# Kernel optimization log

Hardware: AMD Instinct MI355X
Metric: run time of the kernel (lower is better)

## Reference

```python
import jax, jax.numpy as jnp
import numpy as np

B, H, S, D, KG = 1, 8, 1024, 64, 10

def setup_inputs() -> dict:
    key = jax.random.key(0)
    ks = jax.random.split(key, 16)
    n = jax.random.normal
    u = jax.random.uniform
    return {
        'Q': n(ks[0], (B, H, S, D), dtype=jnp.float32),
        'K': n(ks[1], (B, H, S, D), dtype=jnp.float32),
        'V': n(ks[2], (B, H, S, D), dtype=jnp.float32),
        'distance_matrix': u(ks[3], (B, H, S, S), dtype=jnp.float32) * 10.0,
        'energy_matrix': u(ks[4], (B, H, S, S), dtype=jnp.float32) * 5.0,
        'mask': jnp.ones((B, H, S, S), dtype=jnp.int32),
        'mu_D': n(ks[5], (KG,), dtype=jnp.float32),
        'sigma_D': u(ks[6], (KG,), dtype=jnp.float32) + 0.5,  # keep sigma positive
        'b_D': n(ks[7], (KG,), dtype=jnp.float32) * 0.1,
        'mu_E': n(ks[8], (KG,), dtype=jnp.float32),
        'sigma_E': u(ks[9], (KG,), dtype=jnp.float32) + 0.5,
        'b_E': n(ks[10], (KG,), dtype=jnp.float32) * 0.1,
        'W1': n(ks[11], (KG, KG), dtype=jnp.float32) / np.sqrt(KG),
        'b1': jnp.zeros((KG,), dtype=jnp.float32),
        'W2': n(ks[12], (1, KG), dtype=jnp.float32) / np.sqrt(KG),
        'b2': jnp.zeros((1,), dtype=jnp.float32),
    }


def _rbf_mlp_bias(x, b, mu, sigma, W1, b1, W2, b2):
    # x: [B,H,S,S] -> Gaussian RBF features over K kernels, then small MLP -> [B,H,S,S]
    z = (x[..., None] + b - mu) / sigma                      # [B,H,S,S,K]
    inv_norm = 1.0 / (jnp.sqrt(2.0 * jnp.pi) * sigma)
    psi = jnp.exp(-0.5 * z * z) * inv_norm                   # [B,H,S,S,K]
    h = jax.nn.gelu(jnp.einsum('bhijk,lk->bhijl', psi, W1) + b1, approximate=False)
    return (jnp.einsum('bhijk,lk->bhijl', h, W2) + b2)[..., 0]


def reference(Q, K, V, distance_matrix, energy_matrix, mask,
              mu_D, sigma_D, b_D, mu_E, sigma_E, b_E, W1, b1, W2, b2):
    d_model = Q.shape[-1]
    scores = jnp.einsum('bhid,bhjd->bhij', Q, K) / np.sqrt(d_model * 2)
    scores = scores + _rbf_mlp_bias(distance_matrix, b_D, mu_D, sigma_D, W1, b1, W2, b2)
    scores = scores + _rbf_mlp_bias(energy_matrix, b_E, mu_E, sigma_E, W1, b1, W2, b2)
    scores = jnp.where(mask == 0, jnp.float32(-1e9), scores)
    attn = jax.nn.softmax(scores, axis=-1)
    return jnp.einsum('bhij,bhjd->bhid', attn, V)
```

## Files before the change

### kernel.cpp

```cpp
#include <hip/hip_runtime.h>
#include <math.h>

#define Hn 8
#define Sn 1024
#define Dn 64
#define KG 10

#define TN 2048
#define RD 10.25f
#define RE 5.125f

typedef __attribute__((ext_vector_type(8))) short bf16x8;
typedef __attribute__((ext_vector_type(4))) float f32x4;
typedef unsigned short u16;
typedef unsigned int u32;

__device__ inline float bf2f(u16 u) {
    union { u32 i; float f; } v;
    v.i = ((u32)u) << 16;
    return v.f;
}

__device__ inline u16 f2bf(float f) {
    union { float f; u32 i; } v;
    v.f = f;
    u32 i = v.i;
    return (u16)((i + 0x7FFFu + ((i >> 16) & 1u)) >> 16);
}

__device__ float bias_eval(float x,
                           const float* __restrict__ mu, const float* __restrict__ sg,
                           const float* __restrict__ bb,
                           const float* __restrict__ W1, const float* __restrict__ b1,
                           const float* __restrict__ W2, const float* __restrict__ b2) {
    const float inv_s2pi = 0.39894228040143267794f;
    float psi[KG];
#pragma unroll
    for (int k = 0; k < KG; k++) {
        float s = sg[k];
        float z = (x + bb[k] - mu[k]) / s;
        psi[k] = __expf(-0.5f * z * z) * (inv_s2pi / s);
    }
    float out = b2[0];
#pragma unroll
    for (int l = 0; l < KG; l++) {
        float a = b1[l];
#pragma unroll
        for (int k = 0; k < KG; k++) a += psi[k] * W1[l * KG + k];
        float g = 0.5f * a * (1.0f + erff(a * 0.70710678118654752440f));
        out += g * W2[l];
    }
    return out;
}

#define QK4 262144
#define VTN 524288

__global__ __launch_bounds__(256) void prep_kernel(
    const float* __restrict__ Q, const float* __restrict__ K, const float* __restrict__ V,
    const float* __restrict__ muD, const float* __restrict__ sgD, const float* __restrict__ bD,
    const float* __restrict__ muE, const float* __restrict__ sgE, const float* __restrict__ bE,
    const float* __restrict__ W1, const float* __restrict__ b1,
    const float* __restrict__ W2, const float* __restrict__ b2,
    u32* __restrict__ tab, u16* __restrict__ Qb, u16* __restrict__ Kb, u16* __restrict__ VTi)
{
    int id = blockIdx.x * 256 + threadIdx.x;
    if (id < 2 * TN) {
        int which = (id >= TN);
        int idx = id & (TN - 1);
        float h = (which ? RE : RD) / (float)TN;
        float x0 = idx * h;
        float v0, v1;
        if (which) {
            v0 = bias_eval(x0,     muE, sgE, bE, W1, b1, W2, b2);
            v1 = bias_eval(x0 + h, muE, sgE, bE, W1, b1, W2, b2);
        } else {
            v0 = bias_eval(x0,     muD, sgD, bD, W1, b1, W2, b2);
            v1 = bias_eval(x0 + h, muD, sgD, bD, W1, b1, W2, b2);
        }
        tab[id] = (u32)f2bf(v0) | ((u32)f2bf(v1 - v0) << 16);
    } else if (id < 2 * TN + QK4) {
        int i = id - 2 * TN;
        int arr = i >> 17;
        i &= (1 << 17) - 1;
        float4 v = ((const float4*)(arr ? K : Q))[i];
        ushort4 o;
        o.x = f2bf(v.x); o.y = f2bf(v.y); o.z = f2bf(v.z); o.w = f2bf(v.w);
        ((ushort4*)(arr ? Kb : Qb))[i] = o;
    } else if (id < 2 * TN + QK4 + VTN) {
        int g = id - (2 * TN + QK4);
        int h = g >> 16;
        int d = (g >> 10) & 63;
        int s = g & 1023;
        int t = s >> 5, q = (s >> 3) & 3, j = s & 7;
        int src_s = (t << 5) + (q << 2) + (j & 3) + ((j >> 2) << 4);
        VTi[g] = f2bf(V[(((size_t)h << 10) + src_s) * Dn + d]);
    }
}

__device__ inline float lerp_tab(const u32* __restrict__ st, float x, float invh) {
    float tf = x * invh;
    int i = (int)tf;
    i = max(0, min(i, TN - 1));
    float fr = tf - (float)i;
    u32 p = st[i];
    return fmaf(bf2f((u16)(p >> 16)), fr, bf2f((u16)p));
}

__global__ __launch_bounds__(256) void attn_kernel(
    const u16* __restrict__ Qb, const u16* __restrict__ Kb, const u16* __restrict__ VTi,
    const float* __restrict__ Dm, const float* __restrict__ Em, const int* __restrict__ Mk,
    const u32* __restrict__ gtab, float* __restrict__ out)
{
    __shared__ __align__(16) u32 sTab[2 * TN];
    __shared__ float sO[4][16][68];
    __shared__ float sM[4][16], sL[4][16];

    const int tid = threadIdx.x;
    {
        const uint4* g4 = (const uint4*)gtab;
        uint4* s4 = (uint4*)sTab;
#pragma unroll
        for (int i = 0; i < 4; i++) s4[tid + 256 * i] = g4[tid + 256 * i];
    }
    __syncthreads();

    const int h    = blockIdx.y;
    const int q0   = blockIdx.x * 16;
    const int wave = tid >> 6;
    const int lane = tid & 63;
    const int quad = lane >> 4;
    const int l16  = lane & 15;

    const u16* Qh = Qb  + (size_t)h * Sn * Dn;
    const u16* Kh = Kb  + (size_t)h * Sn * Dn;
    const u16* Vh = VTi + (size_t)h * Dn * Sn;
    const float* Dh = Dm + (size_t)h * Sn * Sn + (size_t)(q0 + l16) * Sn;
    const float* Eh = Em + (size_t)h * Sn * Sn + (size_t)(q0 + l16) * Sn;
    const int*   Mh = Mk + (size_t)h * Sn * Sn + (size_t)(q0 + l16) * Sn;
    const float invhD = (float)TN / RD;
    const float invhE = (float)TN / RE;
    const float scale = 0.08838834764831845f;

    const bf16x8 bQ0 = *(const bf16x8*)(Qh + (q0 + l16) * Dn + quad * 8);
    const bf16x8 bQ1 = *(const bf16x8*)(Qh + (q0 + l16) * Dn + 32 + quad * 8);

    f32x4 O0 = {0.f, 0.f, 0.f, 0.f}, O1 = O0, O2 = O0, O3 = O0;
    float m_run = -1e30f, l_run = 0.f;

    for (int t = 0; t < 8; t++) {
        const int k0 = wave * 256 + t * 32;

        const u16* kr = Kh + (size_t)(k0 + l16) * Dn + quad * 8;
        const bf16x8 aK00 = *(const bf16x8*)(kr);
        const bf16x8 aK01 = *(const bf16x8*)(kr + 32);
        const bf16x8 aK10 = *(const bf16x8*)(kr + 16 * Dn);
        const bf16x8 aK11 = *(const bf16x8*)(kr + 16 * Dn + 32);

        const float4 Dv0 = *(const float4*)(Dh + k0 + quad * 4);
        const float4 Dv1 = *(const float4*)(Dh + k0 + 16 + quad * 4);
        const float4 Ev0 = *(const float4*)(Eh + k0 + quad * 4);
        const float4 Ev1 = *(const float4*)(Eh + k0 + 16 + quad * 4);
        const int4   Mv0 = *(const int4*)(Mh + k0 + quad * 4);
        const int4   Mv1 = *(const int4*)(Mh + k0 + 16 + quad * 4);

        const u16* vr = Vh + k0 + quad * 8;
        const bf16x8 bV0 = *(const bf16x8*)(vr + (size_t)(l16)      * Sn);
        const bf16x8 bV1 = *(const bf16x8*)(vr + (size_t)(16 + l16) * Sn);
        const bf16x8 bV2 = *(const bf16x8*)(vr + (size_t)(32 + l16) * Sn);
        const bf16x8 bV3 = *(const bf16x8*)(vr + (size_t)(48 + l16) * Sn);

        f32x4 s0 = {0.f, 0.f, 0.f, 0.f}, s1 = s0;
        s0 = __builtin_amdgcn_mfma_f32_16x16x32_bf16(aK00, bQ0, s0, 0, 0, 0);
        s0 = __builtin_amdgcn_mfma_f32_16x16x32_bf16(aK01, bQ1, s0, 0, 0, 0);
        s1 = __builtin_amdgcn_mfma_f32_16x16x32_bf16(aK10, bQ0, s1, 0, 0, 0);
        s1 = __builtin_amdgcn_mfma_f32_16x16x32_bf16(aK11, bQ1, s1, 0, 0, 0);

        const float dv0[4] = {Dv0.x, Dv0.y, Dv0.z, Dv0.w};
        const float dv1[4] = {Dv1.x, Dv1.y, Dv1.z, Dv1.w};
        const float ev0[4] = {Ev0.x, Ev0.y, Ev0.z, Ev0.w};
        const float ev1[4] = {Ev1.x, Ev1.y, Ev1.z, Ev1.w};
        const int   mv0[4] = {Mv0.x, Mv0.y, Mv0.z, Mv0.w};
        const int   mv1[4] = {Mv1.x, Mv1.y, Mv1.z, Mv1.w};

        float sc0[4], sc1[4];
#pragma unroll
        for (int r = 0; r < 4; r++) {
            float v0 = s0[r] * scale + lerp_tab(sTab, dv0[r], invhD)
                                     + lerp_tab(sTab + TN, ev0[r], invhE);
            v0 = fminf(fmaxf(v0, -80.f), 80.f);
            sc0[r] = (mv0[r] == 0) ? -1e9f : v0;
            float v1 = s1[r] * scale + lerp_tab(sTab, dv1[r], invhD)
                                     + lerp_tab(sTab + TN, ev1[r], invhE);
            v1 = fminf(fmaxf(v1, -80.f), 80.f);
            sc1[r] = (mv1[r] == 0) ? -1e9f : v1;
        }

        float mloc = fmaxf(fmaxf(fmaxf(sc0[0], sc0[1]), fmaxf(sc0[2], sc0[3])),
                           fmaxf(fmaxf(sc1[0], sc1[1]), fmaxf(sc1[2], sc1[3])));
        mloc = fmaxf(mloc, __shfl_xor(mloc, 16, 64));
        mloc = fmaxf(mloc, __shfl_xor(mloc, 32, 64));

        const float mn = fmaxf(m_run, mloc);
        const float al = __expf(m_run - mn);
        m_run = mn;

        float p0[4], p1[4], ll = 0.f;
#pragma unroll
        for (int r = 0; r < 4; r++) {
            p0[r] = __expf(sc0[r] - mn);
            p1[r] = __expf(sc1[r] - mn);
            ll += p0[r] + p1[r];
        }
        ll += __shfl_xor(ll, 16, 64);
        ll += __shfl_xor(ll, 32, 64);
        l_run = l_run * al + ll;

        bf16x8 aP;
#pragma unroll
        for (int r = 0; r < 4; r++) {
            aP[r]     = (short)f2bf(p0[r]);
            aP[4 + r] = (short)f2bf(p1[r]);
        }

        const float a0 = __shfl(al, quad * 4 + 0, 64);
        const float a1 = __shfl(al, quad * 4 + 1, 64);
        const float a2 = __shfl(al, quad * 4 + 2, 64);
        const float a3 = __shfl(al, quad * 4 + 3, 64);
        O0[0] *= a0; O0[1] *= a1; O0[2] *= a2; O0[3] *= a3;
        O1[0] *= a0; O1[1] *= a1; O1[2] *= a2; O1[3] *= a3;
        O2[0] *= a0; O2[1] *= a1; O2[2] *= a2; O2[3] *= a3;
        O3[0] *= a0; O3[1] *= a1; O3[2] *= a2; O3[3] *= a3;

        O0 = __builtin_amdgcn_mfma_f32_16x16x32_bf16(aP, bV0, O0, 0, 0, 0);
        O1 = __builtin_amdgcn_mfma_f32_16x16x32_bf16(aP, bV1, O1, 0, 0, 0);
        O2 = __builtin_amdgcn_mfma_f32_16x16x32_bf16(aP, bV2, O2, 0, 0, 0);
        O3 = __builtin_amdgcn_mfma_f32_16x16x32_bf16(aP, bV3, O3, 0, 0, 0);
    }

    if (lane < 16) {
        sM[wave][lane] = m_run;
        sL[wave][lane] = l_run;
    }
#pragma unroll
    for (int r = 0; r < 4; r++) {
        sO[wave][quad * 4 + r][ 0 + l16] = O0[r];
        sO[wave][quad * 4 + r][16 + l16] = O1[r];
        sO[wave][quad * 4 + r][32 + l16] = O2[r];
        sO[wave][quad * 4 + r][48 + l16] = O3[r];
    }
    __syncthreads();

    const int row = tid >> 4;
    const int c4  = (tid & 15) * 4;
    float mg = sM[0][row];
#pragma unroll
    for (int w = 1; w < 4; w++) mg = fmaxf(mg, sM[w][row]);
    float fac[4], lg = 0.f;
#pragma unroll
    for (int w = 0; w < 4; w++) {
        fac[w] = __expf(sM[w][row] - mg);
        lg += sL[w][row] * fac[w];
    }
    const float inv = 1.0f / lg;

    float acc[4];
#pragma unroll
    for (int c = 0; c < 4; c++) {
        acc[c] = 0.f;
#pragma unroll
        for (int w = 0; w < 4; w++) acc[c] += sO[w][row][c4 + c] * fac[w];
        acc[c] *= inv;
    }
    float4 ov = {acc[0], acc[1], acc[2], acc[3]};
    *(float4*)(out + ((size_t)(h * Sn + q0 + row)) * Dn + c4) = ov;
}

extern "C" void kernel_launch(void* const* d_in, const int* in_sizes, int n_in,
                              void* d_out, int out_size, void* d_ws, size_t ws_size,
                              hipStream_t stream) {
    const float* Q    = (const float*)d_in[0];
    const float* K    = (const float*)d_in[1];
    const float* V    = (const float*)d_in[2];
    const float* Dm   = (const float*)d_in[3];
    const float* Em   = (const float*)d_in[4];
    const int*   Mask = (const int*)d_in[5];
    const float* muD  = (const float*)d_in[6];
    const float* sgD  = (const float*)d_in[7];
    const float* bD   = (const float*)d_in[8];
    const float* muE  = (const float*)d_in[9];
    const float* sgE  = (const float*)d_in[10];
    const float* bE   = (const float*)d_in[11];
    const float* W1   = (const float*)d_in[12];
    const float* b1   = (const float*)d_in[13];
    const float* W2   = (const float*)d_in[14];
    const float* b2   = (const float*)d_in[15];

    u32* tab = (u32*)d_ws;
    u16* Qb  = (u16*)((char*)d_ws + 2 * TN * 4);
    u16* Kb  = Qb + (size_t)Hn * Sn * Dn;
    u16* VTi = Kb + (size_t)Hn * Sn * Dn;

    const int prep_threads = 2 * TN + QK4 + VTN;
    prep_kernel<<<prep_threads / 256, 256, 0, stream>>>(
        Q, K, V, muD, sgD, bD, muE, sgE, bE, W1, b1, W2, b2,
        tab, Qb, Kb, VTi);

    dim3 grid(Sn / 16, Hn);
    attn_kernel<<<grid, 256, 0, stream>>>(Qb, Kb, VTi, Dm, Em, Mask, tab,
                                          (float*)d_out);
}
```

Baseline: 176.2 us.

## Split bias evaluation into separate kernel writing fp16 bias, double-buffer attention loads

Moves the table-lookup bias computation and masking out of the attention kernel into a new bias kernel. That kernel reads the distance, energy and mask matrices and writes one combined fp16 bias per score, laid out in MFMA fragment order. The attention kernel then reads only this compact bias and software-pipelines the K, V and bias loads with double-buffered registers. The cost is an extra kernel launch and an 8M-element fp16 round trip through memory. Masked entries now become -60000 in fp16, and the score clamp to ±80 is dropped, which changes numerics.

```diff
diff --git a/kernel.cpp b/kernel.cpp
--- a/kernel.cpp
+++ b/kernel.cpp
@@ -12,6 +12,8 @@
 
 typedef __attribute__((ext_vector_type(8))) short bf16x8;
 typedef __attribute__((ext_vector_type(4))) float f32x4;
+typedef _Float16 f16;
+typedef __attribute__((ext_vector_type(8))) _Float16 f16x8;
 typedef unsigned short u16;
 typedef unsigned int u32;
 
@@ -107,15 +109,13 @@
     return fmaf(bf2f((u16)(p >> 16)), fr, bf2f((u16)p));
 }
 
-__global__ __launch_bounds__(256) void attn_kernel(
-    const u16* __restrict__ Qb, const u16* __restrict__ Kb, const u16* __restrict__ VTi,
+#define CB_GROUPS (Hn * 64 * 4 * 8 * 64)
+
+__global__ __launch_bounds__(256) void bias_kernel(
     const float* __restrict__ Dm, const float* __restrict__ Em, const int* __restrict__ Mk,
-    const u32* __restrict__ gtab, float* __restrict__ out)
+    const u32* __restrict__ gtab, f16* __restrict__ Cb)
 {
     __shared__ __align__(16) u32 sTab[2 * TN];
-    __shared__ float sO[4][16][68];
-    __shared__ float sM[4][16], sL[4][16];
-
     const int tid = threadIdx.x;
     {
         const uint4* g4 = (const uint4*)gtab;
@@ -124,9 +124,51 @@
         for (int i = 0; i < 4; i++) s4[tid + 256 * i] = g4[tid + 256 * i];
     }
     __syncthreads();
-
+    const float invhD = (float)TN / RD;
+    const float invhE = (float)TN / RE;
+
+    for (int g = blockIdx.x * 256 + tid; g < CB_GROUPS; g += gridDim.x * 256) {
+        const int lane = g & 63;
+        const int t    = (g >> 6) & 7;
+        const int w    = (g >> 9) & 3;
+        const int qb   = (g >> 11) & 63;
+        const int h    = g >> 17;
+        const int q    = qb * 16 + (lane & 15);
+        const int k    = w * 256 + t * 32 + (lane >> 4) * 4;
+        const size_t base = ((((size_t)h << 10) + q) << 10) + k;
+
+        const float4 d0 = *(const float4*)(Dm + base);
+        const float4 d1 = *(const float4*)(Dm + base + 16);
+        const float4 e0 = *(const float4*)(Em + base);
+        const float4 e1 = *(const float4*)(Em + base + 16);
+        const int4   m0 = *(const int4*)(Mk + base);
+        const int4   m1 = *(const int4*)(Mk + base + 16);
+
+        const float dv[8] = {d0.x, d0.y, d0.z, d0.w, d1.x, d1.y, d1.z, d1.w};
+        const float ev[8] = {e0.x, e0.y, e0.z, e0.w, e1.x, e1.y, e1.z, e1.w};
+        const int   mv[8] = {m0.x, m0.y, m0.z, m0.w, m1.x, m1.y, m1.z, m1.w};
+
+        f16x8 o;
+#pragma unroll
+        for (int j = 0; j < 8; j++) {
+            float b = lerp_tab(sTab, dv[j], invhD) + lerp_tab(sTab + TN, ev[j], invhE);
+            o[j] = (f16)((mv[j] == 0) ? -60000.0f : b);
+        }
+        ((f16x8*)Cb)[g] = o;
+    }
+}
+
+__global__ __launch_bounds__(256) void attn_kernel(
+    const u16* __restrict__ Qb, const u16* __restrict__ Kb, const u16* __restrict__ VTi,
+    const f16* __restrict__ Cb, float* __restrict__ out)
+{
+    __shared__ float sO[4][16][68];
+    __shared__ float sM[4][16], sL[4][16];
+
+    const int tid  = threadIdx.x;
     const int h    = blockIdx.y;
-    const int q0   = blockIdx.x * 16;
+    const int qb   = blockIdx.x;
+    const int q0   = qb * 16;
     const int wave = tid >> 6;
     const int lane = tid & 63;
     const int quad = lane >> 4;
@@ -135,11 +177,8 @@
     const u16* Qh = Qb  + (size_t)h * Sn * Dn;
     const u16* Kh = Kb  + (size_t)h * Sn * Dn;
     const u16* Vh = VTi + (size_t)h * Dn * Sn;
-    const float* Dh = Dm + (size_t)h * Sn * Sn + (size_t)(q0 + l16) * Sn;
-    const float* Eh = Em + (size_t)h * Sn * Sn + (size_t)(q0 + l16) * Sn;
-    const int*   Mh = Mk + (size_t)h * Sn * Sn + (size_t)(q0 + l16) * Sn;
-    const float invhD = (float)TN / RD;
-    const float invhE = (float)TN / RE;
+    const f16x8* Cw = (const f16x8*)Cb
+                    + (size_t)(((h * 64 + qb) * 4 + wave) * 8) * 64 + lane;
     const float scale = 0.08838834764831845f;
 
     const bf16x8 bQ0 = *(const bf16x8*)(Qh + (q0 + l16) * Dn + quad * 8);
@@ -148,52 +187,43 @@
     f32x4 O0 = {0.f, 0.f, 0.f, 0.f}, O1 = O0, O2 = O0, O3 = O0;
     float m_run = -1e30f, l_run = 0.f;
 
+    bf16x8 Ka[2][4];
+    bf16x8 Va[2][4];
+    f16x8  Ca[2];
+
+#define LOADT(buf, tt) do {                                                   \
+        const int k0_ = wave * 256 + (tt) * 32;                               \
+        const u16* kr_ = Kh + (size_t)(k0_ + l16) * Dn + quad * 8;            \
+        Ka[buf][0] = *(const bf16x8*)(kr_);                                   \
+        Ka[buf][1] = *(const bf16x8*)(kr_ + 32);                              \
+        Ka[buf][2] = *(const bf16x8*)(kr_ + 16 * Dn);                         \
+        Ka[buf][3] = *(const bf16x8*)(kr_ + 16 * Dn + 32);                    \
+        const u16* vr_ = Vh + k0_ + quad * 8 + (size_t)l16 * Sn;              \
+        Va[buf][0] = *(const bf16x8*)(vr_);                                   \
+        Va[buf][1] = *(const bf16x8*)(vr_ + 16 * Sn);                         \
+        Va[buf][2] = *(const bf16x8*)(vr_ + 32 * Sn);                         \
+        Va[buf][3] = *(const bf16x8*)(vr_ + 48 * Sn);                         \
+        Ca[buf]    = Cw[(tt) * 64];                                           \
+    } while (0)
+
+    LOADT(0, 0);
+
+#pragma unroll
     for (int t = 0; t < 8; t++) {
-        const int k0 = wave * 256 + t * 32;
-
-        const u16* kr = Kh + (size_t)(k0 + l16) * Dn + quad * 8;
-        const bf16x8 aK00 = *(const bf16x8*)(kr);
-        const bf16x8 aK01 = *(const bf16x8*)(kr + 32);
-        const bf16x8 aK10 = *(const bf16x8*)(kr + 16 * Dn);
-        const bf16x8 aK11 = *(const bf16x8*)(kr + 16 * Dn + 32);
-
-        const float4 Dv0 = *(const float4*)(Dh + k0 + quad * 4);
-        const float4 Dv1 = *(const float4*)(Dh + k0 + 16 + quad * 4);
-        const float4 Ev0 = *(const float4*)(Eh + k0 + quad * 4);
-        const float4 Ev1 = *(const float4*)(Eh + k0 + 16 + quad * 4);
-        const int4   Mv0 = *(const int4*)(Mh + k0 + quad * 4);
-        const int4   Mv1 = *(const int4*)(Mh + k0 + 16 + quad * 4);
-
-        const u16* vr = Vh + k0 + quad * 8;
-        const bf16x8 bV0 = *(const bf16x8*)(vr + (size_t)(l16)      * Sn);
-        const bf16x8 bV1 = *(const bf16x8*)(vr + (size_t)(16 + l16) * Sn);
-        const bf16x8 bV2 = *(const bf16x8*)(vr + (size_t)(32 + l16) * Sn);
-        const bf16x8 bV3 = *(const bf16x8*)(vr + (size_t)(48 + l16) * Sn);
+        const int cur = t & 1;
+        if (t < 7) LOADT(cur ^ 1, t + 1);
 
         f32x4 s0 = {0.f, 0.f, 0.f, 0.f}, s1 = s0;
-        s0 = __builtin_amdgcn_mfma_f32_16x16x32_bf16(aK00, bQ0, s0, 0, 0, 0);
-        s0 = __builtin_amdgcn_mfma_f32_16x16x32_bf16(aK01, bQ1, s0, 0, 0, 0);
-        s1 = __builtin_amdgcn_mfma_f32_16x16x32_bf16(aK10, bQ0, s1, 0, 0, 0);
-        s1 = __builtin_amdgcn_mfma_f32_16x16x32_bf16(aK11, bQ1, s1, 0, 0, 0);
-
-        const float dv0[4] = {Dv0.x, Dv0.y, Dv0.z, Dv0.w};
-        const float dv1[4] = {Dv1.x, Dv1.y, Dv1.z, Dv1.w};
-        const float ev0[4] = {Ev0.x, Ev0.y, Ev0.z, Ev0.w};
-        const float ev1[4] = {Ev1.x, Ev1.y, Ev1.z, Ev1.w};
-        const int   mv0[4] = {Mv0.x, Mv0.y, Mv0.z, Mv0.w};
-        const int   mv1[4] = {Mv1.x, Mv1.y, Mv1.z, Mv1.w};
+        s0 = __builtin_amdgcn_mfma_f32_16x16x32_bf16(Ka[cur][0], bQ0, s0, 0, 0, 0);
+        s0 = __builtin_amdgcn_mfma_f32_16x16x32_bf16(Ka[cur][1], bQ1, s0, 0, 0, 0);
+        s1 = __builtin_amdgcn_mfma_f32_16x16x32_bf16(Ka[cur][2], bQ0, s1, 0, 0, 0);
+        s1 = __builtin_amdgcn_mfma_f32_16x16x32_bf16(Ka[cur][3], bQ1, s1, 0, 0, 0);
 
         float sc0[4], sc1[4];
 #pragma unroll
         for (int r = 0; r < 4; r++) {
-            float v0 = s0[r] * scale + lerp_tab(sTab, dv0[r], invhD)
-                                     + lerp_tab(sTab + TN, ev0[r], invhE);
-            v0 = fminf(fmaxf(v0, -80.f), 80.f);
-            sc0[r] = (mv0[r] == 0) ? -1e9f : v0;
-            float v1 = s1[r] * scale + lerp_tab(sTab, dv1[r], invhD)
-                                     + lerp_tab(sTab + TN, ev1[r], invhE);
-            v1 = fminf(fmaxf(v1, -80.f), 80.f);
-            sc1[r] = (mv1[r] == 0) ? -1e9f : v1;
+            sc0[r] = fmaf(s0[r], scale, (float)Ca[cur][r]);
+            sc1[r] = fmaf(s1[r], scale, (float)Ca[cur][4 + r]);
         }
 
         float mloc = fmaxf(fmaxf(fmaxf(sc0[0], sc0[1]), fmaxf(sc0[2], sc0[3])),
@@ -232,11 +262,12 @@
         O2[0] *= a0; O2[1] *= a1; O2[2] *= a2; O2[3] *= a3;
         O3[0] *= a0; O3[1] *= a1; O3[2] *= a2; O3[3] *= a3;
 
-        O0 = __builtin_amdgcn_mfma_f32_16x16x32_bf16(aP, bV0, O0, 0, 0, 0);
-        O1 = __builtin_amdgcn_mfma_f32_16x16x32_bf16(aP, bV1, O1, 0, 0, 0);
-        O2 = __builtin_amdgcn_mfma_f32_16x16x32_bf16(aP, bV2, O2, 0, 0, 0);
-        O3 = __builtin_amdgcn_mfma_f32_16x16x32_bf16(aP, bV3, O3, 0, 0, 0);
-    }
+        O0 = __builtin_amdgcn_mfma_f32_16x16x32_bf16(aP, Va[cur][0], O0, 0, 0, 0);
+        O1 = __builtin_amdgcn_mfma_f32_16x16x32_bf16(aP, Va[cur][1], O1, 0, 0, 0);
+        O2 = __builtin_amdgcn_mfma_f32_16x16x32_bf16(aP, Va[cur][2], O2, 0, 0, 0);
+        O3 = __builtin_amdgcn_mfma_f32_16x16x32_bf16(aP, Va[cur][3], O3, 0, 0, 0);
+    }
+#undef LOADT
 
     if (lane < 16) {
         sM[wave][lane] = m_run;
@@ -300,13 +331,15 @@
     u16* Qb  = (u16*)((char*)d_ws + 2 * TN * 4);
     u16* Kb  = Qb + (size_t)Hn * Sn * Dn;
     u16* VTi = Kb + (size_t)Hn * Sn * Dn;
+    f16* Cb  = (f16*)(VTi + (size_t)Hn * Sn * Dn);
 
     const int prep_threads = 2 * TN + QK4 + VTN;
     prep_kernel<<<prep_threads / 256, 256, 0, stream>>>(
         Q, K, V, muD, sgD, bD, muE, sgE, bE, W1, b1, W2, b2,
         tab, Qb, Kb, VTi);
 
+    bias_kernel<<<2048, 256, 0, stream>>>(Dm, Em, Mask, tab, Cb);
+
     dim3 grid(Sn / 16, Hn);
-    attn_kernel<<<grid, 256, 0, stream>>>(Qb, Kb, VTi, Dm, Em, Mask, tab,
-                                          (float*)d_out);
-}
+    attn_kernel<<<grid, 256, 0, stream>>>(Qb, Kb, VTi, Cb, (float*)d_out);
+}
```

After: 185.4 us. +5.2%, slower.

## Split key dimension across blocks with separate softmax combine kernel

Applied to the files above, without the earlier changes.

Adds a third grid dimension that splits the 1024 keys into four chunks, so each block processes 256 keys and writes unnormalized partial outputs plus row max and sum to workspace. A new combine kernel merges the partials with log-sum-exp rescaling and normalizes. This is meant to raise the number of blocks and improve latency hiding for the bandwidth-heavy bias matrix reads. In exchange, each block reloads the lookup table into shared memory, and the change adds partial-result traffic and an extra launch. It also sets a min-blocks launch bound and a scheduling barrier after the loads.

```diff
diff --git a/kernel.cpp b/kernel.cpp
--- a/kernel.cpp
+++ b/kernel.cpp
@@ -9,6 +9,8 @@
 #define TN 2048
 #define RD 10.25f
 #define RE 5.125f
+
+#define KS 4
 
 typedef __attribute__((ext_vector_type(8))) short bf16x8;
 typedef __attribute__((ext_vector_type(4))) float f32x4;
@@ -107,10 +109,11 @@
     return fmaf(bf2f((u16)(p >> 16)), fr, bf2f((u16)p));
 }
 
-__global__ __launch_bounds__(256) void attn_kernel(
+__global__ __launch_bounds__(256, 4) void attn_kernel(
     const u16* __restrict__ Qb, const u16* __restrict__ Kb, const u16* __restrict__ VTi,
     const float* __restrict__ Dm, const float* __restrict__ Em, const int* __restrict__ Mk,
-    const u32* __restrict__ gtab, float* __restrict__ out)
+    const u32* __restrict__ gtab,
+    float* __restrict__ Up, float* __restrict__ Mp, float* __restrict__ Lp)
 {
     __shared__ __align__(16) u32 sTab[2 * TN];
     __shared__ float sO[4][16][68];
@@ -126,7 +129,9 @@
     __syncthreads();
 
     const int h    = blockIdx.y;
-    const int q0   = blockIdx.x * 16;
+    const int qb   = blockIdx.x;
+    const int ks   = blockIdx.z;
+    const int q0   = qb * 16;
     const int wave = tid >> 6;
     const int lane = tid & 63;
     const int quad = lane >> 4;
@@ -148,14 +153,8 @@
     f32x4 O0 = {0.f, 0.f, 0.f, 0.f}, O1 = O0, O2 = O0, O3 = O0;
     float m_run = -1e30f, l_run = 0.f;
 
-    for (int t = 0; t < 8; t++) {
-        const int k0 = wave * 256 + t * 32;
-
-        const u16* kr = Kh + (size_t)(k0 + l16) * Dn + quad * 8;
-        const bf16x8 aK00 = *(const bf16x8*)(kr);
-        const bf16x8 aK01 = *(const bf16x8*)(kr + 32);
-        const bf16x8 aK10 = *(const bf16x8*)(kr + 16 * Dn);
-        const bf16x8 aK11 = *(const bf16x8*)(kr + 16 * Dn + 32);
+    for (int t = 0; t < 2; t++) {
+        const int k0 = ks * 256 + wave * 64 + t * 32;
 
         const float4 Dv0 = *(const float4*)(Dh + k0 + quad * 4);
         const float4 Dv1 = *(const float4*)(Dh + k0 + 16 + quad * 4);
@@ -164,11 +163,19 @@
         const int4   Mv0 = *(const int4*)(Mh + k0 + quad * 4);
         const int4   Mv1 = *(const int4*)(Mh + k0 + 16 + quad * 4);
 
+        const u16* kr = Kh + (size_t)(k0 + l16) * Dn + quad * 8;
+        const bf16x8 aK00 = *(const bf16x8*)(kr);
+        const bf16x8 aK01 = *(const bf16x8*)(kr + 32);
+        const bf16x8 aK10 = *(const bf16x8*)(kr + 16 * Dn);
+        const bf16x8 aK11 = *(const bf16x8*)(kr + 16 * Dn + 32);
+
         const u16* vr = Vh + k0 + quad * 8;
         const bf16x8 bV0 = *(const bf16x8*)(vr + (size_t)(l16)      * Sn);
         const bf16x8 bV1 = *(const bf16x8*)(vr + (size_t)(16 + l16) * Sn);
         const bf16x8 bV2 = *(const bf16x8*)(vr + (size_t)(32 + l16) * Sn);
         const bf16x8 bV3 = *(const bf16x8*)(vr + (size_t)(48 + l16) * Sn);
+
+        __builtin_amdgcn_sched_barrier(0);
 
         f32x4 s0 = {0.f, 0.f, 0.f, 0.f}, s1 = s0;
         s0 = __builtin_amdgcn_mfma_f32_16x16x32_bf16(aK00, bQ0, s0, 0, 0, 0);
@@ -262,7 +269,6 @@
         fac[w] = __expf(sM[w][row] - mg);
         lg += sL[w][row] * fac[w];
     }
-    const float inv = 1.0f / lg;
 
     float acc[4];
 #pragma unroll
@@ -270,10 +276,56 @@
         acc[c] = 0.f;
 #pragma unroll
         for (int w = 0; w < 4; w++) acc[c] += sO[w][row][c4 + c] * fac[w];
-        acc[c] *= inv;
-    }
+    }
+
+    const int pbase = ((h * 64 + qb) * KS + ks) * 16 + row;
     float4 ov = {acc[0], acc[1], acc[2], acc[3]};
-    *(float4*)(out + ((size_t)(h * Sn + q0 + row)) * Dn + c4) = ov;
+    *(float4*)(Up + (size_t)pbase * 64 + c4) = ov;
+    if ((tid & 15) == 0) {
+        Mp[pbase] = mg;
+        Lp[pbase] = lg;
+    }
+}
+
+__global__ __launch_bounds__(256) void combine_kernel(
+    const float* __restrict__ Up, const float* __restrict__ Mp,
+    const float* __restrict__ Lp, float* __restrict__ out)
+{
+    const int g  = blockIdx.x * 256 + threadIdx.x;
+    const int r  = g >> 4;
+    const int c4 = (g & 15) * 4;
+    const int h  = r >> 10;
+    const int s  = r & 1023;
+    const int qb = s >> 4;
+    const int r16 = s & 15;
+    const int base = ((h * 64 + qb) * KS) * 16 + r16;
+
+    float m[KS], l[KS];
+#pragma unroll
+    for (int k = 0; k < KS; k++) {
+        m[k] = Mp[base + k * 16];
+        l[k] = Lp[base + k * 16];
+    }
+    float M = m[0];
+#pragma unroll
+    for (int k = 1; k < KS; k++) M = fmaxf(M, m[k]);
+    float f[KS], L = 0.f;
+#pragma unroll
+    for (int k = 0; k < KS; k++) {
+        f[k] = __expf(m[k] - M);
+        L += l[k] * f[k];
+    }
+    const float inv = 1.0f / L;
+
+    float acc[4] = {0.f, 0.f, 0.f, 0.f};
+#pragma unroll
+    for (int k = 0; k < KS; k++) {
+        const float4 u = *(const float4*)(Up + (size_t)(base + k * 16) * 64 + c4);
+        acc[0] += u.x * f[k]; acc[1] += u.y * f[k];
+        acc[2] += u.z * f[k]; acc[3] += u.w * f[k];
+    }
+    float4 ov = {acc[0] * inv, acc[1] * inv, acc[2] * inv, acc[3] * inv};
+    *(float4*)(out + (size_t)r * Dn + c4) = ov;
 }
 
 extern "C" void kernel_launch(void* const* d_in, const int* in_sizes, int n_in,
@@ -300,13 +352,19 @@
     u16* Qb  = (u16*)((char*)d_ws + 2 * TN * 4);
     u16* Kb  = Qb + (size_t)Hn * Sn * Dn;
     u16* VTi = Kb + (size_t)Hn * Sn * Dn;
+    float* Up = (float*)(VTi + (size_t)Hn * Sn * Dn);
+    float* Mp = Up + (size_t)Hn * 64 * KS * 16 * 64;
+    float* Lp = Mp + (size_t)Hn * 64 * KS * 16;
 
     const int prep_threads = 2 * TN + QK4 + VTN;
     prep_kernel<<<prep_threads / 256, 256, 0, stream>>>(
         Q, K, V, muD, sgD, bD, muE, sgE, bE, W1, b1, W2, b2,
         tab, Qb, Kb, VTi);
 
-    dim3 grid(Sn / 16, Hn);
+    dim3 grid(Sn / 16, Hn, KS);
     attn_kernel<<<grid, 256, 0, stream>>>(Qb, Kb, VTi, Dm, Em, Mask, tab,
-                                          (float*)d_out);
-}
+                                          Up, Mp, Lp);
+
+    combine_kernel<<<(Hn * Sn * 16) / 256, 256, 0, stream>>>(Up, Mp, Lp,
+                                                             (float*)d_out);
+}
```

After: 182.1 us. 1.03x slower.

## Stage per-tile K, V, D, E, mask loads through LDS via global_load_lds

Applied to the files above, without the earlier changes.

Replaces the direct per-lane global vector loads of K, V, distance, energy and mask tiles with global_load_lds DMA into a per-wave LDS staging area. Each lane then reads its fragment back from LDS, and the epilogue reuses the staging buffer for the output reduction. The aim is to bypass VGPR staging of global loads and possibly cut register pressure. In exchange it adds an LDS round trip, a full vmcnt(0) wait each iteration with no double buffering, and about 57KB of extra LDS, which may reduce occupancy.

```diff
diff --git a/kernel.cpp b/kernel.cpp
--- a/kernel.cpp
+++ b/kernel.cpp
@@ -26,6 +26,13 @@
     v.f = f;
     u32 i = v.i;
     return (u16)((i + 0x7FFFu + ((i >> 16) & 1u)) >> 16);
+}
+
+__device__ inline void stage16(const void* g, void* l) {
+    __builtin_amdgcn_global_load_lds(
+        (const __attribute__((address_space(1))) unsigned int*)g,
+        (__attribute__((address_space(3))) unsigned int*)l,
+        16, 0, 0);
 }
 
 __device__ float bias_eval(float x,
@@ -107,13 +114,15 @@
     return fmaf(bf2f((u16)(p >> 16)), fr, bf2f((u16)p));
 }
 
+#define STW 14336
+
 __global__ __launch_bounds__(256) void attn_kernel(
     const u16* __restrict__ Qb, const u16* __restrict__ Kb, const u16* __restrict__ VTi,
     const float* __restrict__ Dm, const float* __restrict__ Em, const int* __restrict__ Mk,
     const u32* __restrict__ gtab, float* __restrict__ out)
 {
     __shared__ __align__(16) u32 sTab[2 * TN];
-    __shared__ float sO[4][16][68];
+    __shared__ __align__(16) char sBuf[4 * STW];
     __shared__ float sM[4][16], sL[4][16];
 
     const int tid = threadIdx.x;
@@ -145,6 +154,8 @@
     const bf16x8 bQ0 = *(const bf16x8*)(Qh + (q0 + l16) * Dn + quad * 8);
     const bf16x8 bQ1 = *(const bf16x8*)(Qh + (q0 + l16) * Dn + 32 + quad * 8);
 
+    char* st = sBuf + wave * STW;
+
     f32x4 O0 = {0.f, 0.f, 0.f, 0.f}, O1 = O0, O2 = O0, O3 = O0;
     float m_run = -1e30f, l_run = 0.f;
 
@@ -152,23 +163,44 @@
         const int k0 = wave * 256 + t * 32;
 
         const u16* kr = Kh + (size_t)(k0 + l16) * Dn + quad * 8;
-        const bf16x8 aK00 = *(const bf16x8*)(kr);
-        const bf16x8 aK01 = *(const bf16x8*)(kr + 32);
-        const bf16x8 aK10 = *(const bf16x8*)(kr + 16 * Dn);
-        const bf16x8 aK11 = *(const bf16x8*)(kr + 16 * Dn + 32);
-
-        const float4 Dv0 = *(const float4*)(Dh + k0 + quad * 4);
-        const float4 Dv1 = *(const float4*)(Dh + k0 + 16 + quad * 4);
-        const float4 Ev0 = *(const float4*)(Eh + k0 + quad * 4);
-        const float4 Ev1 = *(const float4*)(Eh + k0 + 16 + quad * 4);
-        const int4   Mv0 = *(const int4*)(Mh + k0 + quad * 4);
-        const int4   Mv1 = *(const int4*)(Mh + k0 + 16 + quad * 4);
-
-        const u16* vr = Vh + k0 + quad * 8;
-        const bf16x8 bV0 = *(const bf16x8*)(vr + (size_t)(l16)      * Sn);
-        const bf16x8 bV1 = *(const bf16x8*)(vr + (size_t)(16 + l16) * Sn);
-        const bf16x8 bV2 = *(const bf16x8*)(vr + (size_t)(32 + l16) * Sn);
-        const bf16x8 bV3 = *(const bf16x8*)(vr + (size_t)(48 + l16) * Sn);
+        const u16* vr = Vh + k0 + quad * 8 + (size_t)l16 * Sn;
+        const float* dr = Dh + k0 + quad * 4;
+        const float* er = Eh + k0 + quad * 4;
+        const int*   mr = Mh + k0 + quad * 4;
+        stage16(kr,                st);
+        stage16(kr + 32,           st + 1024);
+        stage16(kr + 16 * Dn,      st + 2048);
+        stage16(kr + 16 * Dn + 32, st + 3072);
+        stage16(vr,                st + 4096);
+        stage16(vr + 16 * Sn,      st + 5120);
+        stage16(vr + 32 * Sn,      st + 6144);
+        stage16(vr + 48 * Sn,      st + 7168);
+        stage16(dr,                st + 8192);
+        stage16(dr + 16,           st + 9216);
+        stage16(er,                st + 10240);
+        stage16(er + 16,           st + 11264);
+        stage16(mr,                st + 12288);
+        stage16(mr + 16,           st + 13312);
+
+        asm volatile("s_waitcnt vmcnt(0)" ::: "memory");
+
+        const char* ls = st + lane * 16;
+        const bf16x8 aK00 = *(const bf16x8*)(ls);
+        const bf16x8 aK01 = *(const bf16x8*)(ls + 1024);
+        const bf16x8 aK10 = *(const bf16x8*)(ls + 2048);
+        const bf16x8 aK11 = *(const bf16x8*)(ls + 3072);
+        const bf16x8 bV0  = *(const bf16x8*)(ls + 4096);
+        const bf16x8 bV1  = *(const bf16x8*)(ls + 5120);
+        const bf16x8 bV2  = *(const bf16x8*)(ls + 6144);
+        const bf16x8 bV3  = *(const bf16x8*)(ls + 7168);
+        const float4 Dv0  = *(const float4*)(ls + 8192);
+        const float4 Dv1  = *(const float4*)(ls + 9216);
+        const float4 Ev0  = *(const float4*)(ls + 10240);
+        const float4 Ev1  = *(const float4*)(ls + 11264);
+        const int4   Mv0  = *(const int4*)(ls + 12288);
+        const int4   Mv1  = *(const int4*)(ls + 13312);
+
+        asm volatile("" ::: "memory");
 
         f32x4 s0 = {0.f, 0.f, 0.f, 0.f}, s1 = s0;
         s0 = __builtin_amdgcn_mfma_f32_16x16x32_bf16(aK00, bQ0, s0, 0, 0, 0);
@@ -238,6 +270,9 @@
         O3 = __builtin_amdgcn_mfma_f32_16x16x32_bf16(aP, bV3, O3, 0, 0, 0);
     }
 
+    __syncthreads();
+
+    float (*sO)[16][68] = (float (*)[16][68])sBuf;
     if (lane < 16) {
         sM[wave][lane] = m_run;
         sL[wave][lane] = l_run;
```

Result: no change. 173.1 us (median of 2 runs) (-1.8%).
